# Kernel optimization log

Hardware: AMD Instinct MI355X
Metric: run time of the kernel (lower is better)

Reference implementation:

```python
import jax, jax.numpy as jnp
import numpy as np

N1, N2, C, H = 512, 512, 256, 512

def setup_inputs() -> dict:
    key = jax.random.key(0)
    ks = jax.random.split(key, 8)
    std = 0.01
    return {
        "X": jax.random.normal(ks[0], (N1, C), dtype=jnp.float32),
        "Y": jax.random.normal(ks[1], (N2, C), dtype=jnp.float32),
        "W_sr": jax.random.normal(ks[2], (C, C), dtype=jnp.float32) * std,   # project_sr.weight
        "W_tg": jax.random.normal(ks[3], (C, C), dtype=jnp.float32) * std,   # project_tg.weight
        "W1": jax.random.normal(ks[4], (H, 2 * C), dtype=jnp.float32) * std, # fc_M[0].weight [512,512]
        "b1": jnp.zeros((H,), dtype=jnp.float32),                            # fc_M[0].bias
        "w2": jax.random.normal(ks[5], (1, H), dtype=jnp.float32) * std,     # fc_M[2].weight [1,512]
        "b2": jnp.zeros((1,), dtype=jnp.float32),                            # fc_M[2].bias
    }

def reference(X, Y, W_sr, W_tg, W1, b1, w2, b2):
    # Projections (Linear without bias): x @ W.T
    Xp = X @ W_sr.T  # [N1, C]
    Yp = Y @ W_tg.T  # [N2, C]
    # fc_M first layer acts on concat([X_k, Y_k], -1); split W1 into the
    # halves that multiply Xp and Yp respectively (mathematically identical
    # to materializing the [N1,N2,2C] concat, but avoids it).
    W1x, W1y = W1[:, :C], W1[:, C:]
    hx = Xp @ W1x.T                     # [N1, H]
    hy = Yp @ W1y.T                     # [N2, H]
    Hid = jax.nn.relu(hx[:, None, :] + hy[None, :, :] + b1)  # [N1, N2, H]
    M = Hid @ w2[0] + b2[0]             # [N1, N2]  (squeeze of last dim 1)
    return M
```

## Files before the change

### kernel.cpp

```cpp
#include <hip/hip_runtime.h>


typedef _Float16 h2 __attribute__((ext_vector_type(2)));
typedef _Float16 h4 __attribute__((ext_vector_type(4)));
typedef _Float16 h8 __attribute__((ext_vector_type(8)));

__global__ __launch_bounds__(128) void gemm1_f16(
    const float* __restrict__ A0, const float* __restrict__ A1,
    const float* __restrict__ B0, const float* __restrict__ B1,
    _Float16* __restrict__ C0, _Float16* __restrict__ C1)
{
    const int z = blockIdx.z;
    const float* A = z ? A1 : A0;
    const float* B = z ? B1 : B0;
    _Float16* Cc   = z ? C1 : C0;

    __shared__ _Float16 As2[16 * 72];
    __shared__ _Float16 Bs2[16 * 72];

    const int t  = threadIdx.x;
    const int m0 = blockIdx.x * 32;
    const int n0 = blockIdx.y * 32;
    const int ti = t >> 4;
    const int tj = t & 15;

    float acc[4][2] = {};

    for (int kt = 0; kt < 256; kt += 32) {
        #pragma unroll
        for (int r = 0; r < 2; r++) {
            const int id  = t + r * 128;
            const int m   = id >> 3;
            const int k4  = (id & 7) * 4;
            const int kp0 = k4 >> 1;
            float4 v = *(const float4*)&A[(m0 + m) * 256 + kt + k4];
            h2 lo = {(_Float16)v.x, (_Float16)v.y};
            h2 hi = {(_Float16)v.z, (_Float16)v.w};
            *(h2*)&As2[kp0 * 72 + 2 * m]       = lo;
            *(h2*)&As2[(kp0 + 1) * 72 + 2 * m] = hi;
        }
        #pragma unroll
        for (int r = 0; r < 2; r++) {
            const int id  = t + r * 128;
            const int n   = id >> 3;
            const int k4  = (id & 7) * 4;
            const int kp0 = k4 >> 1;
            float4 v = *(const float4*)&B[(n0 + n) * 256 + kt + k4];
            h2 lo = {(_Float16)v.x, (_Float16)v.y};
            h2 hi = {(_Float16)v.z, (_Float16)v.w};
            *(h2*)&Bs2[kp0 * 72 + 2 * n]       = lo;
            *(h2*)&Bs2[(kp0 + 1) * 72 + 2 * n] = hi;
        }
        __syncthreads();

        #pragma unroll 8
        for (int kp = 0; kp < 16; kp++) {
            h8 a = *(const h8*)&As2[kp * 72 + 8 * ti];
            h4 b = *(const h4*)&Bs2[kp * 72 + 4 * tj];
            const h2* ap = (const h2*)&a;
            const h2* bp = (const h2*)&b;
            #pragma unroll
            for (int mi = 0; mi < 4; mi++)
                #pragma unroll
                for (int nj = 0; nj < 2; nj++)
                    acc[mi][nj] = __builtin_amdgcn_fdot2(ap[mi], bp[nj],
                                                         acc[mi][nj], false);
        }
        __syncthreads();
    }

    #pragma unroll
    for (int mi = 0; mi < 4; mi++) {
        const int m = m0 + 4 * ti + mi;
        h2 r = {(_Float16)acc[mi][0], (_Float16)acc[mi][1]};
        *(h2*)&Cc[m * 256 + n0 + 2 * tj] = r;
    }
}

__global__ __launch_bounds__(128) void gemm2_f16(
    const _Float16* __restrict__ A0, const _Float16* __restrict__ A1,
    const float* __restrict__ B0, const float* __restrict__ B1,
    _Float16* __restrict__ C0, _Float16* __restrict__ C1,
    const float* __restrict__ bias1)
{
    const int z = blockIdx.z;
    const _Float16* A = z ? A1 : A0;
    const float* B    = z ? B1 : B0;
    _Float16* Cc      = z ? C1 : C0;
    const float* bias = z ? bias1 : nullptr;

    __shared__ _Float16 As2[16 * 72];
    __shared__ _Float16 Bs2[16 * 136];

    const int t  = threadIdx.x;
    const int m0 = blockIdx.x * 32;
    const int n0 = blockIdx.y * 64;
    const int ti = t >> 4;
    const int tj = t & 15;

    float acc[4][4] = {};

    for (int kt = 0; kt < 256; kt += 32) {
        {
            const int m   = t >> 2;
            const int k8  = (t & 3) * 8;
            const int kp0 = k8 >> 1;
            h8 v = *(const h8*)&A[(m0 + m) * 256 + kt + k8];
            #pragma unroll
            for (int i = 0; i < 4; i++) {
                h2 p = {v[2 * i], v[2 * i + 1]};
                *(h2*)&As2[(kp0 + i) * 72 + 2 * m] = p;
            }
        }
        #pragma unroll
        for (int r = 0; r < 4; r++) {
            const int id  = t + r * 128;
            const int n   = id >> 3;
            const int k4  = (id & 7) * 4;
            const int kp0 = k4 >> 1;
            float4 v = *(const float4*)&B[(n0 + n) * 512 + kt + k4];
            h2 lo = {(_Float16)v.x, (_Float16)v.y};
            h2 hi = {(_Float16)v.z, (_Float16)v.w};
            *(h2*)&Bs2[kp0 * 136 + 2 * n]       = lo;
            *(h2*)&Bs2[(kp0 + 1) * 136 + 2 * n] = hi;
        }
        __syncthreads();

        #pragma unroll 8
        for (int kp = 0; kp < 16; kp++) {
            h8 a = *(const h8*)&As2[kp * 72 + 8 * ti];
            h8 b = *(const h8*)&Bs2[kp * 136 + 8 * tj];
            const h2* ap = (const h2*)&a;
            const h2* bp = (const h2*)&b;
            #pragma unroll
            for (int mi = 0; mi < 4; mi++)
                #pragma unroll
                for (int nj = 0; nj < 4; nj++)
                    acc[mi][nj] = __builtin_amdgcn_fdot2(ap[mi], bp[nj],
                                                         acc[mi][nj], false);
        }
        __syncthreads();
    }

    float4 bv = {0.f, 0.f, 0.f, 0.f};
    if (bias) bv = *(const float4*)&bias[n0 + 4 * tj];
    #pragma unroll
    for (int mi = 0; mi < 4; mi++) {
        const int m = m0 + 4 * ti + mi;
        h4 r = {(_Float16)(acc[mi][0] + bv.x), (_Float16)(acc[mi][1] + bv.y),
                (_Float16)(acc[mi][2] + bv.z), (_Float16)(acc[mi][3] + bv.w)};
        *(h4*)&Cc[m * 512 + n0 + 4 * tj] = r;
    }
}

__global__ __launch_bounds__(256) void affinity_core(
    const _Float16* __restrict__ hx, const _Float16* __restrict__ hy,
    const float* __restrict__ w2, _Float16* __restrict__ partial)
{
    __shared__ __align__(16) _Float16 xs[64 * 72];
    __shared__ __align__(16) _Float16 ys[64 * 72];
    __shared__ __align__(16) _Float16 ws2[64];

    const int t  = threadIdx.x;
    const int i0 = blockIdx.x * 64;
    const int j0 = blockIdx.y * 64;
    const int h0 = blockIdx.z * 64;
    const int ti = t / 16;
    const int tj = t % 16;

    #pragma unroll
    for (int s = 0; s < 2; s++) {
        const int id = t + s * 256;
        const int r  = id >> 3;
        const int c8 = (id & 7) * 8;
        *(float4*)&xs[r * 72 + c8] = *(const float4*)&hx[(i0 + r) * 512 + h0 + c8];
        *(float4*)&ys[r * 72 + c8] = *(const float4*)&hy[(j0 + r) * 512 + h0 + c8];
    }
    if (t < 64) ws2[t] = (_Float16)w2[h0 + t];
    __syncthreads();

    float acc[4][4] = {};
    const _Float16* xr = xs + ti * 72;
    const _Float16* yr = ys + tj * 72;
    const h2 hz = {(_Float16)0.f, (_Float16)0.f};

    #pragma unroll 2
    for (int g = 0; g < 8; g++) {
        const int ho = g * 8;
        h8 w = *(const h8*)&ws2[ho];
        h8 x[4], y[4];
        #pragma unroll
        for (int m = 0; m < 4; m++) x[m] = *(const h8*)&xr[m * (16 * 72) + ho];
        #pragma unroll
        for (int n = 0; n < 4; n++) y[n] = *(const h8*)&yr[n * (16 * 72) + ho];
        const h2* wp = (const h2*)&w;
        #pragma unroll
        for (int m = 0; m < 4; m++) {
            const h2* xp = (const h2*)&x[m];
            #pragma unroll
            for (int n = 0; n < 4; n++) {
                const h2* yp = (const h2*)&y[n];
                float a = acc[m][n];
                #pragma unroll
                for (int p = 0; p < 4; p++) {
                    h2 s = xp[p] + yp[p];
                    s = __builtin_elementwise_max(s, hz);
                    a = __builtin_amdgcn_fdot2(s, wp[p], a, false);
                }
                acc[m][n] = a;
            }
        }
    }

    _Float16* p = partial + blockIdx.z * (512 * 512);
    #pragma unroll
    for (int m = 0; m < 4; m++) {
        #pragma unroll
        for (int n = 0; n < 4; n++) {
            p[(i0 + ti + 16 * m) * 512 + (j0 + tj + 16 * n)] = (_Float16)acc[m][n];
        }
    }
}

__global__ __launch_bounds__(256) void reduce8(
    const _Float16* __restrict__ partial, const float* __restrict__ b2,
    float* __restrict__ out)
{
    const int idx = (blockIdx.x * 256 + threadIdx.x) * 4;
    const float bb = b2[0];
    float4 r = {bb, bb, bb, bb};
    #pragma unroll
    for (int s = 0; s < 8; s++) {
        h4 p = *(const h4*)&partial[s * 262144 + idx];
        r.x += (float)p[0]; r.y += (float)p[1];
        r.z += (float)p[2]; r.w += (float)p[3];
    }
    *(float4*)&out[idx] = r;
}

extern "C" void kernel_launch(void* const* d_in, const int* in_sizes, int n_in,
                              void* d_out, int out_size, void* d_ws, size_t ws_size,
                              hipStream_t stream) {
    const float* X    = (const float*)d_in[0];
    const float* Y    = (const float*)d_in[1];
    const float* W_sr = (const float*)d_in[2];
    const float* W_tg = (const float*)d_in[3];
    const float* W1   = (const float*)d_in[4];
    const float* b1   = (const float*)d_in[5];
    const float* w2   = (const float*)d_in[6];
    const float* b2   = (const float*)d_in[7];

    float* ws = (float*)d_ws;
    _Float16* Xp      = (_Float16*)ws;
    _Float16* Yp      = (_Float16*)(ws + 65536);
    _Float16* hx      = (_Float16*)(ws + 131072);
    _Float16* hy      = (_Float16*)(ws + 262144);
    _Float16* partial = (_Float16*)(ws + 393216);
    float* out = (float*)d_out;

    gemm1_f16<<<dim3(16, 8, 2), 128, 0, stream>>>(
        X, Y, W_sr, W_tg, Xp, Yp);
    gemm2_f16<<<dim3(16, 8, 2), 128, 0, stream>>>(
        Xp, Yp, W1, W1 + 256, hx, hy, b1);
    affinity_core<<<dim3(8, 8, 8), 256, 0, stream>>>(hx, hy, w2, partial);
    reduce8<<<256, 256, 0, stream>>>(partial, b2, out);
}
```

Baseline: 105.4 us.

## Replace partial buffer and reduce kernel with atomics; prefetch GEMM tiles into registers

The affinity kernel now atomically adds its H-slice partial sums straight into the fp32 output, which gemm1 first fills with the b2 bias. This removes the fp16 partial buffer writes, the separate reduce kernel and one launch. Both small GEMMs also load the next K tile into registers while computing on the current one, to hide global load latency. The cost is 8-way atomic contention on every output element and a nondeterministic summation order.

```diff
diff --git a/kernel.cpp b/kernel.cpp
--- a/kernel.cpp
+++ b/kernel.cpp
@@ -8,7 +8,8 @@
 __global__ __launch_bounds__(128) void gemm1_f16(
     const float* __restrict__ A0, const float* __restrict__ A1,
     const float* __restrict__ B0, const float* __restrict__ B1,
-    _Float16* __restrict__ C0, _Float16* __restrict__ C1)
+    _Float16* __restrict__ C0, _Float16* __restrict__ C1,
+    const float* __restrict__ b2, float* __restrict__ out)
 {
     const int z = blockIdx.z;
     const float* A = z ? A1 : A0;
@@ -24,7 +25,24 @@
     const int ti = t >> 4;
     const int tj = t & 15;
 
+    {
+        const int bid = blockIdx.x + 16 * (blockIdx.y + 8 * blockIdx.z);
+        const float bb = b2[0];
+        float4 f = {bb, bb, bb, bb};
+        float* o = out + bid * 1024 + t * 8;
+        *(float4*)o = f;
+        *(float4*)(o + 4) = f;
+    }
+
     float acc[4][2] = {};
+
+    float4 va[2], vb[2];
+    #pragma unroll
+    for (int r = 0; r < 2; r++) {
+        const int id = t + r * 128;
+        va[r] = *(const float4*)&A[(m0 + (id >> 3)) * 256 + (id & 7) * 4];
+        vb[r] = *(const float4*)&B[(n0 + (id >> 3)) * 256 + (id & 7) * 4];
+    }
 
     for (int kt = 0; kt < 256; kt += 32) {
         #pragma unroll
@@ -33,25 +51,25 @@
             const int m   = id >> 3;
             const int k4  = (id & 7) * 4;
             const int kp0 = k4 >> 1;
-            float4 v = *(const float4*)&A[(m0 + m) * 256 + kt + k4];
-            h2 lo = {(_Float16)v.x, (_Float16)v.y};
-            h2 hi = {(_Float16)v.z, (_Float16)v.w};
-            *(h2*)&As2[kp0 * 72 + 2 * m]       = lo;
-            *(h2*)&As2[(kp0 + 1) * 72 + 2 * m] = hi;
-        }
-        #pragma unroll
-        for (int r = 0; r < 2; r++) {
-            const int id  = t + r * 128;
-            const int n   = id >> 3;
-            const int k4  = (id & 7) * 4;
-            const int kp0 = k4 >> 1;
-            float4 v = *(const float4*)&B[(n0 + n) * 256 + kt + k4];
-            h2 lo = {(_Float16)v.x, (_Float16)v.y};
-            h2 hi = {(_Float16)v.z, (_Float16)v.w};
-            *(h2*)&Bs2[kp0 * 72 + 2 * n]       = lo;
-            *(h2*)&Bs2[(kp0 + 1) * 72 + 2 * n] = hi;
-        }
-        __syncthreads();
+            h2 alo = {(_Float16)va[r].x, (_Float16)va[r].y};
+            h2 ahi = {(_Float16)va[r].z, (_Float16)va[r].w};
+            *(h2*)&As2[kp0 * 72 + 2 * m]       = alo;
+            *(h2*)&As2[(kp0 + 1) * 72 + 2 * m] = ahi;
+            h2 blo = {(_Float16)vb[r].x, (_Float16)vb[r].y};
+            h2 bhi = {(_Float16)vb[r].z, (_Float16)vb[r].w};
+            *(h2*)&Bs2[kp0 * 72 + 2 * m]       = blo;
+            *(h2*)&Bs2[(kp0 + 1) * 72 + 2 * m] = bhi;
+        }
+        __syncthreads();
+
+        if (kt < 224) {
+            #pragma unroll
+            for (int r = 0; r < 2; r++) {
+                const int id = t + r * 128;
+                va[r] = *(const float4*)&A[(m0 + (id >> 3)) * 256 + kt + 32 + (id & 7) * 4];
+                vb[r] = *(const float4*)&B[(n0 + (id >> 3)) * 256 + kt + 32 + (id & 7) * 4];
+            }
+        }
 
         #pragma unroll 8
         for (int kp = 0; kp < 16; kp++) {
@@ -100,15 +118,27 @@
 
     float acc[4][4] = {};
 
+    h8 va;
+    float4 vb[4];
+    {
+        const int m  = t >> 2;
+        const int k8 = (t & 3) * 8;
+        va = *(const h8*)&A[(m0 + m) * 256 + k8];
+    }
+    #pragma unroll
+    for (int r = 0; r < 4; r++) {
+        const int id = t + r * 128;
+        vb[r] = *(const float4*)&B[(n0 + (id >> 3)) * 512 + (id & 7) * 4];
+    }
+
     for (int kt = 0; kt < 256; kt += 32) {
         {
             const int m   = t >> 2;
             const int k8  = (t & 3) * 8;
             const int kp0 = k8 >> 1;
-            h8 v = *(const h8*)&A[(m0 + m) * 256 + kt + k8];
             #pragma unroll
             for (int i = 0; i < 4; i++) {
-                h2 p = {v[2 * i], v[2 * i + 1]};
+                h2 p = {va[2 * i], va[2 * i + 1]};
                 *(h2*)&As2[(kp0 + i) * 72 + 2 * m] = p;
             }
         }
@@ -118,13 +148,23 @@
             const int n   = id >> 3;
             const int k4  = (id & 7) * 4;
             const int kp0 = k4 >> 1;
-            float4 v = *(const float4*)&B[(n0 + n) * 512 + kt + k4];
-            h2 lo = {(_Float16)v.x, (_Float16)v.y};
-            h2 hi = {(_Float16)v.z, (_Float16)v.w};
+            h2 lo = {(_Float16)vb[r].x, (_Float16)vb[r].y};
+            h2 hi = {(_Float16)vb[r].z, (_Float16)vb[r].w};
             *(h2*)&Bs2[kp0 * 136 + 2 * n]       = lo;
             *(h2*)&Bs2[(kp0 + 1) * 136 + 2 * n] = hi;
         }
         __syncthreads();
+
+        if (kt < 224) {
+            const int m  = t >> 2;
+            const int k8 = (t & 3) * 8;
+            va = *(const h8*)&A[(m0 + m) * 256 + kt + 32 + k8];
+            #pragma unroll
+            for (int r = 0; r < 4; r++) {
+                const int id = t + r * 128;
+                vb[r] = *(const float4*)&B[(n0 + (id >> 3)) * 512 + kt + 32 + (id & 7) * 4];
+            }
+        }
 
         #pragma unroll 8
         for (int kp = 0; kp < 16; kp++) {
@@ -155,7 +195,7 @@
 
 __global__ __launch_bounds__(256) void affinity_core(
     const _Float16* __restrict__ hx, const _Float16* __restrict__ hy,
-    const float* __restrict__ w2, _Float16* __restrict__ partial)
+    const float* __restrict__ w2, float* __restrict__ out)
 {
     __shared__ __align__(16) _Float16 xs[64 * 72];
     __shared__ __align__(16) _Float16 ys[64 * 72];
@@ -212,30 +252,14 @@
         }
     }
 
-    _Float16* p = partial + blockIdx.z * (512 * 512);
     #pragma unroll
     for (int m = 0; m < 4; m++) {
         #pragma unroll
         for (int n = 0; n < 4; n++) {
-            p[(i0 + ti + 16 * m) * 512 + (j0 + tj + 16 * n)] = (_Float16)acc[m][n];
-        }
-    }
-}
-
-__global__ __launch_bounds__(256) void reduce8(
-    const _Float16* __restrict__ partial, const float* __restrict__ b2,
-    float* __restrict__ out)
-{
-    const int idx = (blockIdx.x * 256 + threadIdx.x) * 4;
-    const float bb = b2[0];
-    float4 r = {bb, bb, bb, bb};
-    #pragma unroll
-    for (int s = 0; s < 8; s++) {
-        h4 p = *(const h4*)&partial[s * 262144 + idx];
-        r.x += (float)p[0]; r.y += (float)p[1];
-        r.z += (float)p[2]; r.w += (float)p[3];
-    }
-    *(float4*)&out[idx] = r;
+            atomicAdd(&out[(i0 + ti + 16 * m) * 512 + (j0 + tj + 16 * n)],
+                      acc[m][n]);
+        }
+    }
 }
 
 extern "C" void kernel_launch(void* const* d_in, const int* in_sizes, int n_in,
@@ -251,17 +275,15 @@
     const float* b2   = (const float*)d_in[7];
 
     float* ws = (float*)d_ws;
-    _Float16* Xp      = (_Float16*)ws;
-    _Float16* Yp      = (_Float16*)(ws + 65536);
-    _Float16* hx      = (_Float16*)(ws + 131072);
-    _Float16* hy      = (_Float16*)(ws + 262144);
-    _Float16* partial = (_Float16*)(ws + 393216);
+    _Float16* Xp = (_Float16*)ws;
+    _Float16* Yp = (_Float16*)(ws + 65536);
+    _Float16* hx = (_Float16*)(ws + 131072);
+    _Float16* hy = (_Float16*)(ws + 262144);
     float* out = (float*)d_out;
 
     gemm1_f16<<<dim3(16, 8, 2), 128, 0, stream>>>(
-        X, Y, W_sr, W_tg, Xp, Yp);
+        X, Y, W_sr, W_tg, Xp, Yp, b2, out);
     gemm2_f16<<<dim3(16, 8, 2), 128, 0, stream>>>(
         Xp, Yp, W1, W1 + 256, hx, hy, b1);
-    affinity_core<<<dim3(8, 8, 8), 256, 0, stream>>>(hx, hy, w2, partial);
-    reduce8<<<256, 256, 0, stream>>>(partial, b2, out);
-}
+    affinity_core<<<dim3(8, 8, 8), 256, 0, stream>>>(hx, hy, w2, out);
+}
```

Result: faster. 98.58 us (-6.5%).
